# Kernel optimization log

Measured on AMD Instinct MI355X. Metric: run time of the kernel, lower is better.

Reference implementation:

```python
import jax, jax.numpy as jnp
import numpy as np
from jax import lax

DIM = 384
HEADS = 8
CROP = 8


def conv2d(x, w, groups=1, pad=0):
    return lax.conv_general_dilated(
        x, w, (1, 1), ((pad, pad), (pad, pad)),
        dimension_numbers=("NCHW", "OIHW", "NCHW"),
        feature_group_count=groups)


def l2norm(x, axis):
    # F.normalize: x / max(||x||_2, 1e-12)
    n = jnp.sqrt(jnp.sum(x * x, axis=axis, keepdims=True))
    return x / jnp.maximum(n, 1e-12)


def masked_softmax(a, k):
    # top-k mask via k-th largest threshold (equivalent to scatter mask for
    # continuous-valued scores), then softmax with -inf fill.
    kth = lax.top_k(a, k)[0][..., -1:]
    return jax.nn.softmax(jnp.where(a >= kth, a, -jnp.inf), axis=-1)


def setup_inputs() -> dict:
    key = jax.random.key(0)
    ks = jax.random.split(key, 5)
    b, c, h, w = 2, DIM, 128, 128
    x = jax.random.normal(ks[0], (b, c, h, w), dtype=jnp.float32)
    w_qkv = jax.random.normal(ks[1], (3 * c, c, 1, 1), dtype=jnp.float32) * 0.02
    w_dw = jax.random.normal(ks[2], (3 * c, 1, 3, 3), dtype=jnp.float32) * 0.02
    w_proj = jax.random.normal(ks[3], (c, c, 1, 1), dtype=jnp.float32) * 0.02
    temperature = jnp.ones((HEADS, 1, 1), dtype=jnp.float32)
    a = jnp.full((1,), 0.2, dtype=jnp.float32)
    return {"x": x, "w_qkv": w_qkv, "w_dw": w_dw, "w_proj": w_proj,
            "temperature": temperature, "attn1": a, "attn2": a,
            "attn3": a, "attn4": a}


def reference(x, w_qkv, w_dw, w_proj, temperature, attn1, attn2, attn3, attn4):
    b, c, h, w = x.shape
    heads, crop = HEADS, CROP
    ch = c // heads                      # per-head channels C
    N = crop * crop                      # window tokens

    qkv = conv2d(conv2d(x, w_qkv), w_dw, groups=3 * c, pad=1)
    q, k, v = jnp.split(qkv, 3, axis=1)

    def to_heads(t):                     # b (head c) h w -> b head c (h w)
        return t.reshape(b, heads, ch, h * w)

    def to_win(t):                       # imgtowindows on (b, head, c, h, w)
        t = t.reshape(b, heads, ch, h // crop, crop, w // crop, crop)
        t = jnp.transpose(t, (0, 1, 3, 5, 4, 6, 2))
        return t.reshape(-1, heads, N, ch)

    qc, kc, vc = to_heads(q), to_heads(k), to_heads(v)
    qs = to_win(q.reshape(b, heads, ch, h, w))
    ks_ = to_win(k.reshape(b, heads, ch, h, w))
    vs = to_win(v.reshape(b, heads, ch, h, w))

    qc, kc = l2norm(qc, -1), l2norm(kc, -1)
    qs, ks_ = l2norm(qs, -1), l2norm(ks_, -1)

    cattn = jnp.einsum("bhcn,bhdn->bhcd", qc, kc) * temperature  # (b,H,C,C)
    sattn = jnp.einsum("bhnc,bhmc->bhnm", qs, ks_) * temperature  # (B',H,N,N)

    cks = [ch // 2, (ch * 2) // 3, (ch * 3) // 4, (ch * 4) // 5]
    sks = [N // 2, (N * 2) // 3, (N * 3) // 4, (N * 4) // 5]
    wts = [attn1, attn2, attn3, attn4]

    cout = sum((masked_softmax(cattn, kk) @ vc) * wt for kk, wt in zip(cks, wts))
    sout = sum((masked_softmax(sattn, kk) @ vs) * wt for kk, wt in zip(sks, wts))

    # windowstoimg (replicates torch's contiguous view/reshape semantics)
    sout = sout.reshape(b, heads, h, w, ch)
    sout = jnp.transpose(sout, (0, 1, 4, 2, 3)).reshape(b, heads, ch, h * w)

    out = (sout + cout).reshape(b, c, h, w)
    return conv2d(out, w_proj)
```

## Files before the change

### kernel.cpp

```cpp
#include <hip/hip_runtime.h>
#include <hip/hip_bf16.h>


#define HW 16384
#define CDIM 384
#define NHEADS 8
#define CH 48
#define NCHUNK 128

typedef __hip_bfloat16 bf16;
typedef __attribute__((ext_vector_type(8))) short short8;
typedef __attribute__((ext_vector_type(4))) float f32x4;

static __device__ __forceinline__ unsigned short f2bf_bits(float v) {
  bf16 b = __float2bfloat16(v);
  return __builtin_bit_cast(unsigned short, b);
}
static __device__ __forceinline__ float bfbits2f(unsigned short u) {
  return __bfloat162float(__builtin_bit_cast(bf16, u));
}

template <int CTRL>
static __device__ __forceinline__ float dppf(float x) {
  return __builtin_bit_cast(
      float, __builtin_amdgcn_update_dpp(0, __builtin_bit_cast(int, x), CTRL,
                                         0xF, 0xF, true));
}

__global__ __launch_bounds__(256) void decomp_w(const float* __restrict__ src,
                                                unsigned short* __restrict__ h,
                                                unsigned short* __restrict__ l, int n) {
  int i = blockIdx.x * 256 + threadIdx.x;
  if (i >= n) return;
  float v = src[i];
  unsigned short hb = f2bf_bits(v);
  h[i] = hb;
  l[i] = f2bf_bits(v - bfbits2f(hb));
}

__global__ __launch_bounds__(256) void transpose_frag(const float* __restrict__ src,
                                                      short8* __restrict__ dh,
                                                      short8* __restrict__ dl) {
  const int o = blockIdx.x * 256 + threadIdx.x;
  const int ptile = o / 768;
  const int rem = o - ptile * 768;
  const int kc = rem >> 6, lane = rem & 63;
  const int p = ptile * 16 + (lane & 15);
  const int kb = kc * 32 + (lane >> 4) * 8;
  short8 hh, ll;
#pragma unroll
  for (int j = 0; j < 8; j++) {
    float v = src[(size_t)(kb + j) * HW + p];
    unsigned short hb = f2bf_bits(v);
    hh[j] = (short)hb;
    ll[j] = (short)f2bf_bits(v - bfbits2f(hb));
  }
  dh[o] = hh;
  dl[o] = ll;
}

__global__ __launch_bounds__(256, 4) void gemm_mfma(const unsigned short* __restrict__ Wh,
                                                    const unsigned short* __restrict__ Wl,
                                                    const short8* __restrict__ Xh,
                                                    const short8* __restrict__ Xl,
                                                    float* __restrict__ Out) {
  const int tid = threadIdx.x;
  const int wave = tid >> 6, lane = tid & 63;
  const int lm = lane & 15, lq = lane >> 4;
  const int g = blockIdx.y * 128 + blockIdx.x;
  const int xcd = g & 7, i = g >> 3;
  const int bx = xcd * 16 + (i & 15);
  const int by = i >> 4;
  const int p0 = bx * 128;
  const int oc0 = by * 64;
  const int pt0 = bx * 8 + wave * 2;
  f32x4 acc[4][2] = {};
#pragma unroll
  for (int kc = 0; kc < 12; kc++) {
    short8 ah[4], al[4], bh[2], bl[2];
#pragma unroll
    for (int mt = 0; mt < 4; mt++) {
      const size_t off = (size_t)(oc0 + mt * 16 + lm) * 384 + kc * 32 + lq * 8;
      ah[mt] = *reinterpret_cast<const short8*>(Wh + off);
      al[mt] = *reinterpret_cast<const short8*>(Wl + off);
    }
#pragma unroll
    for (int nt = 0; nt < 2; nt++) {
      const size_t idx = (size_t)((pt0 + nt) * 12 + kc) * 64 + lane;
      bh[nt] = Xh[idx];
      bl[nt] = Xl[idx];
    }
#pragma unroll
    for (int mt = 0; mt < 4; mt++)
#pragma unroll
      for (int nt = 0; nt < 2; nt++) {
        acc[mt][nt] = __builtin_amdgcn_mfma_f32_16x16x32_bf16(ah[mt], bh[nt], acc[mt][nt], 0, 0, 0);
        acc[mt][nt] = __builtin_amdgcn_mfma_f32_16x16x32_bf16(ah[mt], bl[nt], acc[mt][nt], 0, 0, 0);
        acc[mt][nt] = __builtin_amdgcn_mfma_f32_16x16x32_bf16(al[mt], bh[nt], acc[mt][nt], 0, 0, 0);
      }
  }
#pragma unroll
  for (int mt = 0; mt < 4; mt++)
#pragma unroll
    for (int nt = 0; nt < 2; nt++)
#pragma unroll
      for (int r = 0; r < 4; r++) {
        const int oc = oc0 + mt * 16 + lq * 4 + r;
        const int p = p0 + (wave * 2 + nt) * 16 + lm;
        Out[(size_t)oc * HW + p] = acc[mt][nt][r];
      }
}

__global__ __launch_bounds__(256) void dwconv3(const float* __restrict__ A,
                                               const float* __restrict__ wdw,
                                               float* __restrict__ Bq) {
  const int e = blockIdx.x * 256 + threadIdx.x;
  const int x4 = e & 31;
  const int y = (e >> 5) & 127;
  const int ch = e >> 12;
  const int x0 = x4 << 2;
  float w[9];
#pragma unroll
  for (int t = 0; t < 9; t++) w[t] = wdw[ch * 9 + t];
  const float* Ap = A + (size_t)ch * HW;
  float4 acc = {0.f, 0.f, 0.f, 0.f};
#pragma unroll
  for (int ky = 0; ky < 3; ky++) {
    const int yy = y + ky - 1;
    if (yy < 0 || yy > 127) continue;
    const float* row = Ap + yy * 128;
    const float4 c = *(const float4*)(row + x0);
    const float l = (x4 == 0) ? 0.f : row[x0 - 1];
    const float r = (x4 == 31) ? 0.f : row[x0 + 4];
    const float w0 = w[ky * 3], w1 = w[ky * 3 + 1], w2 = w[ky * 3 + 2];
    acc.x += w0 * l + w1 * c.x + w2 * c.y;
    acc.y += w0 * c.x + w1 * c.y + w2 * c.z;
    acc.z += w0 * c.y + w1 * c.z + w2 * c.w;
    acc.w += w0 * c.z + w1 * c.w + w2 * r;
  }
  *(float4*)(Bq + (size_t)e * 4) = acc;
}

__global__ __launch_bounds__(256) void chan_norms(const float* __restrict__ Bq,
                                                  float* __restrict__ inv) {
  const int row = blockIdx.x;
  const float4* base = (const float4*)(Bq + (size_t)row * HW);
  const int tid = threadIdx.x;
  float s = 0.f;
  for (int p = tid; p < HW / 4; p += 256) {
    const float4 v = base[p];
    s += v.x * v.x + v.y * v.y + v.z * v.z + v.w * v.w;
  }
  for (int o = 32; o; o >>= 1) s += __shfl_xor(s, o);
  __shared__ float red[4];
  if ((tid & 63) == 0) red[tid >> 6] = s;
  __syncthreads();
  if (tid == 0) {
    float t = red[0] + red[1] + red[2] + red[3];
    inv[row] = 1.f / fmaxf(sqrtf(t), 1e-12f);
  }
}

__global__ __launch_bounds__(256, 3) void cattn_partial(const float* __restrict__ Bq,
                                                        float* __restrict__ part) {
  __shared__ __align__(16) float qs[48 * 132];
  __shared__ __align__(16) float ks2[48 * 132];
  const int tid = threadIdx.x;
  const int chunk = blockIdx.x, h = blockIdx.y;
  const int p0 = chunk * 128;
#pragma unroll
  for (int i = 0; i < 12; i++) {
    const int s4 = tid + i * 256;
    const int t = s4 >= 1536;
    const int r4 = s4 - t * 1536;
    const int cc = r4 >> 5;
    const int px = (r4 & 31) << 2;
    const float4 v4 = *(const float4*)(Bq + (size_t)(t * CDIM + h * CH + cc) * HW + p0 + px);
    *(float4*)((t ? ks2 : qs) + cc * 132 + px) = v4;
  }
  __syncthreads();
  const int tx = tid & 15, ty = tid >> 4;
  const float* qb = qs + (ty * 3) * 132;
  const float* kb = ks2 + (tx * 3) * 132;
  float acc[3][3] = {};
  for (int pl = 0; pl < 128; pl += 4) {
    float4 qv[3], kv[3];
#pragma unroll
    for (int ii = 0; ii < 3; ii++) qv[ii] = *(const float4*)(qb + ii * 132 + pl);
#pragma unroll
    for (int jj = 0; jj < 3; jj++) kv[jj] = *(const float4*)(kb + jj * 132 + pl);
#pragma unroll
    for (int ii = 0; ii < 3; ii++)
#pragma unroll
      for (int jj = 0; jj < 3; jj++)
        acc[ii][jj] += qv[ii].x * kv[jj].x + qv[ii].y * kv[jj].y +
                       qv[ii].z * kv[jj].z + qv[ii].w * kv[jj].w;
  }
  float* rp = part + (size_t)(h * NCHUNK + chunk) * 2304;
#pragma unroll
  for (int ii = 0; ii < 3; ii++)
#pragma unroll
    for (int jj = 0; jj < 3; jj++)
      rp[(ty * 3 + ii) * 48 + tx * 3 + jj] = acc[ii][jj];
}

__global__ __launch_bounds__(64) void chan_softmax(
    const float* __restrict__ part, const float* __restrict__ inv,
    const float* __restrict__ temp, const float* __restrict__ a1,
    const float* __restrict__ a2, const float* __restrict__ a3,
    const float* __restrict__ a4, float* __restrict__ W48) {
  const int blk = blockIdx.x;
  const int i = blk % 48;
  const int h = blk / 48;
  const int lane = threadIdx.x;
  const float t = temp[h];
  float a = -3.0e38f;
  if (lane < 48) {
    const float* pp = part + (size_t)h * NCHUNK * 2304 + i * 48 + lane;
    float r = 0.f;
#pragma unroll 8
    for (int c = 0; c < NCHUNK; c++) r += pp[(size_t)c * 2304];
    a = t * inv[h * CH + i] * inv[CDIM + h * CH + lane] * r;
  }
  float m = a;
  for (int o = 32; o; o >>= 1) m = fmaxf(m, __shfl_xor(m, o));
  float e = (lane < 48) ? expf(a - m) : 0.f;
  int gt = 0;
  for (int j = 0; j < 48; j++) {
    float vj = __shfl(a, j);
    gt += (vj > a) ? 1 : 0;
  }
  const int ksel[4] = {24, 32, 36, 38};
  const float wts[4] = {a1[0], a2[0], a3[0], a4[0]};
  float coef = 0.f;
#pragma unroll
  for (int kk = 0; kk < 4; kk++) {
    float sel = (gt < ksel[kk]) ? e : 0.f;
    for (int o = 32; o; o >>= 1) sel += __shfl_xor(sel, o);
    if (gt < ksel[kk]) coef += wts[kk] / sel;
  }
  if (lane < 48) W48[(size_t)blk * 48 + lane] = e * coef;
}

__global__ __launch_bounds__(256) void cout_kernel(const float* __restrict__ W48,
                                                   const float* __restrict__ Bq,
                                                   float* __restrict__ Cbuf) {
  __shared__ __align__(16) float Wl[2304];
  const int tid = threadIdx.x;
  const int h = blockIdx.y;
  const float* wsrc = W48 + (size_t)h * 2304;
  for (int s = tid; s < 2304; s += 256) Wl[s] = wsrc[s];
  __syncthreads();
  const int p = blockIdx.x * 64 + (tid & 63);
  const int ig = tid >> 6;
  const float* vbase = Bq + (size_t)(2 * CDIM + h * CH) * HW + p;
  float acc[12] = {};
  for (int j0 = 0; j0 < 48; j0 += 4) {
    float vj[4];
#pragma unroll
    for (int q = 0; q < 4; q++) vj[q] = vbase[(size_t)(j0 + q) * HW];
#pragma unroll
    for (int ii = 0; ii < 12; ii++) {
      const float4 w4 = *reinterpret_cast<const float4*>(&Wl[(ig * 12 + ii) * 48 + j0]);
      acc[ii] += w4.x * vj[0] + w4.y * vj[1] + w4.z * vj[2] + w4.w * vj[3];
    }
  }
  float* obase = Cbuf + (size_t)(h * CH + ig * 12) * HW + p;
#pragma unroll
  for (int ii = 0; ii < 12; ii++) obase[(size_t)ii * HW] += acc[ii];
}

static __device__ __forceinline__ void conv_frag_k(int f, const float* kRaw,
                                                   short8* KFh, short8* KFl) {
  int nt, ks, slot;
  if (f < 256) { nt = f >> 6; ks = 0; slot = f & 63; }
  else { const int g2 = f - 256; nt = g2 >> 5; ks = 1; slot = g2 & 31; }
  const int tok = nt * 16 + (slot & 15);
  const int ch0 = ks * 32 + (slot >> 4) * 8;
  const float* src = kRaw + tok * 49 + ch0;
  short8 hh, ll;
#pragma unroll
  for (int j = 0; j < 8; j++) {
    const float v = src[j];
    const unsigned short hb = f2bf_bits(v);
    hh[j] = (short)hb;
    ll[j] = (short)f2bf_bits(v - bfbits2f(hb));
  }
  KFh[f] = hh;
  KFl[f] = ll;
}

__global__ __launch_bounds__(256, 4) void spatial_kernel(
    const float* __restrict__ Bq, const float* __restrict__ temp,
    const float* __restrict__ a1, const float* __restrict__ a2,
    const float* __restrict__ a3, const float* __restrict__ a4,
    float* __restrict__ Cbuf) {
  __shared__ __align__(16) char smem[40192];
  float* qRaw = (float*)smem;
  float* kRaw = (float*)(smem + 12544);
  short8* KFh = (short8*)(smem + 25088);
  short8* KFl = (short8*)(smem + 31232);
  float* S_lds = (float*)smem;
  unsigned short* VTh = (unsigned short*)(smem + 16640);
  unsigned short* VTl = (unsigned short*)(smem + 23552);
  bf16* Pl = (bf16*)(smem + 30464);
  float* O_lds = (float*)smem;
  float* invQ = (float*)(smem + 39680);
  float* invK = (float*)(smem + 39936);

  const int bid = blockIdx.x;
  const int wid = ((bid & 7) << 8) | (bid >> 3);
  const int wx = wid & 15, wy = (wid >> 4) & 15;
  const int head = wid >> 8;
  const int tid = threadIdx.x;
  const int lane = tid & 63, w = tid >> 6;
  const int lm = lane & 15, lq = lane >> 4;
  const int ybase = wy * 8, xbase = wx * 8;
  const size_t hb = (size_t)(head * CH) * HW;

#pragma unroll
  for (int i = 0; i < 6; i++) {
    const int s4 = tid + i * 256;
    const int t = s4 >= 768;
    const int r4 = s4 - t * 768;
    const int cc = r4 >> 4, nq = r4 & 15;
    const int n = nq * 4;
    const int y = ybase + (n >> 3), x = xbase + (n & 7);
    const float4 v4 = *(const float4*)(Bq + (size_t)(t * CDIM) * HW + hb +
                                       (size_t)cc * HW + y * 128 + x);
    float* dst = (t ? kRaw : qRaw) + n * 49 + cc;
    dst[0] = v4.x; dst[49] = v4.y; dst[98] = v4.z; dst[147] = v4.w;
  }
  __syncthreads();

  float4 vv[3];
#pragma unroll
  for (int i = 0; i < 3; i++) {
    const int e4 = tid + i * 256;
    const int cc = e4 >> 4, n = (e4 & 15) * 4;
    const int y = ybase + (n >> 3), x = xbase + (n & 7);
    vv[i] = *(const float4*)(Bq + (size_t)(2 * CDIM) * HW + hb +
                             (size_t)cc * HW + y * 128 + x);
  }

  if (tid < 128) {
    const int t = tid >> 6, n = tid & 63;
    const float* src = (t ? kRaw : qRaw) + n * 49;
    float ssum = 0.f;
#pragma unroll
    for (int cc = 0; cc < 48; cc++) { float v = src[cc]; ssum += v * v; }
    const float iv = 1.f / fmaxf(sqrtf(ssum), 1e-12f);
    if (t) invK[n] = iv; else invQ[n] = iv * temp[head];
  }

  conv_frag_k(tid, kRaw, KFh, KFl);
  if (tid < 128) conv_frag_k(256 + tid, kRaw, KFh, KFl);

  short8 qh[2], ql[2];
#pragma unroll
  for (int ks = 0; ks < 2; ks++) {
    const int ch0 = ks * 32 + lq * 8;
    const float* qp = qRaw + (w * 16 + lm) * 49 + ch0;
#pragma unroll
    for (int j = 0; j < 8; j++) {
      const float v = (ch0 < 48) ? qp[j] : 0.f;
      const unsigned short hbts = f2bf_bits(v);
      qh[ks][j] = (short)hbts;
      ql[ks][j] = (short)f2bf_bits(v - bfbits2f(hbts));
    }
  }
  __syncthreads();

  f32x4 sacc[4] = {};
#pragma unroll
  for (int nt = 0; nt < 4; nt++) {
    const short8 kh0 = KFh[nt * 64 + lane];
    const short8 kl0 = KFl[nt * 64 + lane];
    sacc[nt] = __builtin_amdgcn_mfma_f32_16x16x32_bf16(qh[0], kh0, sacc[nt], 0, 0, 0);
    sacc[nt] = __builtin_amdgcn_mfma_f32_16x16x32_bf16(qh[0], kl0, sacc[nt], 0, 0, 0);
    sacc[nt] = __builtin_amdgcn_mfma_f32_16x16x32_bf16(ql[0], kh0, sacc[nt], 0, 0, 0);
    short8 kh1 = {0, 0, 0, 0, 0, 0, 0, 0}, kl1 = {0, 0, 0, 0, 0, 0, 0, 0};
    if (lane < 32) { kh1 = KFh[256 + nt * 32 + lane]; kl1 = KFl[256 + nt * 32 + lane]; }
    sacc[nt] = __builtin_amdgcn_mfma_f32_16x16x32_bf16(qh[1], kh1, sacc[nt], 0, 0, 0);
    sacc[nt] = __builtin_amdgcn_mfma_f32_16x16x32_bf16(qh[1], kl1, sacc[nt], 0, 0, 0);
    sacc[nt] = __builtin_amdgcn_mfma_f32_16x16x32_bf16(ql[1], kh1, sacc[nt], 0, 0, 0);
  }

  float iqv[4];
#pragma unroll
  for (int r = 0; r < 4; r++) iqv[r] = invQ[w * 16 + lq * 4 + r];
#pragma unroll
  for (int nt = 0; nt < 4; nt++) {
    const float ik = invK[nt * 16 + lm];
#pragma unroll
    for (int r = 0; r < 4; r++)
      S_lds[(w * 16 + lq * 4 + r) * 65 + nt * 16 + lm] = sacc[nt][r] * iqv[r] * ik;
  }
  __syncthreads();

#pragma unroll
  for (int i = 0; i < 3; i++) {
    const int e4 = tid + i * 256;
    const int cc = e4 >> 4, n = (e4 & 15) * 4;
    const float v0 = vv[i].x, v1 = vv[i].y, v2 = vv[i].z, v3 = vv[i].w;
    const unsigned short h0 = f2bf_bits(v0), h1 = f2bf_bits(v1),
                         h2 = f2bf_bits(v2), h3 = f2bf_bits(v3);
    const ushort4 hh = {h0, h1, h2, h3};
    const ushort4 ll = {f2bf_bits(v0 - bfbits2f(h0)), f2bf_bits(v1 - bfbits2f(h1)),
                        f2bf_bits(v2 - bfbits2f(h2)), f2bf_bits(v3 - bfbits2f(h3))};
    *(ushort4*)(VTh + cc * 72 + n) = hh;
    *(ushort4*)(VTl + cc * 72 + n) = ll;
  }

  const float wts[4] = {a1[0], a2[0], a3[0], a4[0]};
  const int sidx[4] = {32, 22, 16, 13};
#pragma unroll 4
  for (int rr = 0; rr < 16; rr++) {
    const int row = w * 16 + rr;
    const float a = S_lds[row * 65 + lane];
    float s = a;
#pragma unroll
    for (int k2 = 2; k2 <= 64; k2 <<= 1) {
#pragma unroll
      for (int j = k2 >> 1; j > 0; j >>= 1) {
        float o;
        if (j == 1)      o = dppf<0xB1>(s);
        else if (j == 2) o = dppf<0x4E>(s);
        else if (j == 8) o = dppf<0x128>(s);
        else             o = __shfl_xor(s, j);
        const bool up = ((lane & k2) == 0);
        const bool lower = ((lane & j) == 0);
        const float mn = fminf(s, o), mx = fmaxf(s, o);
        s = (lower == up) ? mn : mx;
      }
    }
    const float m = __shfl(s, 63);
    float v = __expf(s - m);
    v += dppf<0x101>(v);
    v += dppf<0x102>(v);
    v += dppf<0x104>(v);
    v += dppf<0x108>(v);
    const float t1 = __shfl(v, 16), t2 = __shfl(v, 32), t3 = __shfl(v, 48);
    const float beyond =
        (lq == 0) ? (t1 + t2 + t3) : (lq == 1) ? (t2 + t3) : (lq == 2) ? t3 : 0.f;
    const float suf = v + beyond;
    const float e = __expf(a - m);
    float coef = 0.f;
#pragma unroll
    for (int kk = 0; kk < 4; kk++) {
      const float tk = __shfl(s, sidx[kk]);
      const float Sk = __shfl(suf, sidx[kk]);
      if (a >= tk) coef += wts[kk] * __builtin_amdgcn_rcpf(Sk);
    }
    Pl[row * 72 + lane] = __float2bfloat16(e * coef);
  }
  __syncthreads();

  short8 pa[2];
#pragma unroll
  for (int ks = 0; ks < 2; ks++)
    pa[ks] = *reinterpret_cast<const short8*>(&Pl[(w * 16 + lm) * 72 + ks * 32 + lq * 8]);
  f32x4 oacc[3] = {};
#pragma unroll
  for (int nt = 0; nt < 3; nt++) {
    const int chv = nt * 16 + lm;
#pragma unroll
    for (int ks = 0; ks < 2; ks++) {
      const short8 vh = *reinterpret_cast<const short8*>(VTh + chv * 72 + ks * 32 + lq * 8);
      const short8 vl = *reinterpret_cast<const short8*>(VTl + chv * 72 + ks * 32 + lq * 8);
      oacc[nt] = __builtin_amdgcn_mfma_f32_16x16x32_bf16(pa[ks], vh, oacc[nt], 0, 0, 0);
      oacc[nt] = __builtin_amdgcn_mfma_f32_16x16x32_bf16(pa[ks], vl, oacc[nt], 0, 0, 0);
    }
  }
#pragma unroll
  for (int nt = 0; nt < 3; nt++)
#pragma unroll
    for (int r = 0; r < 4; r++)
      O_lds[(nt * 16 + lm) * 65 + w * 16 + lq * 4 + r] = oacc[nt][r];
  __syncthreads();

  const int y_out = wy * 8 + (wx >> 1);
  const int x0 = (wx & 1) * 64;
#pragma unroll
  for (int i = 0; i < 3; i++) {
    const int s4 = tid + i * 256;
    const int cc = s4 >> 4, n = (s4 & 15) * 4;
    const float* op = O_lds + cc * 65 + n;
    const float4 o4 = {op[0], op[1], op[2], op[3]};
    *(float4*)(Cbuf + ((size_t)(head * CH + cc) * 128 + y_out) * 128 + x0 + n) = o4;
  }
}

extern "C" void kernel_launch(void* const* d_in, const int* in_sizes, int n_in,
                              void* d_out, int out_size, void* d_ws, size_t ws_size,
                              hipStream_t stream) {
  const float* x = (const float*)d_in[0];
  const float* w_qkv = (const float*)d_in[1];
  const float* w_dw = (const float*)d_in[2];
  const float* w_proj = (const float*)d_in[3];
  const float* temp = (const float*)d_in[4];
  const float* a1 = (const float*)d_in[5];
  const float* a2 = (const float*)d_in[6];
  const float* a3 = (const float*)d_in[7];
  const float* a4 = (const float*)d_in[8];
  float* out = (float*)d_out;

  char* ws = (char*)d_ws;
  float* cattn_part = (float*)ws;
  float* W48 = (float*)(ws + 9437184);
  float* inv = (float*)(ws + 9510912);
  unsigned short* wqkv_h = (unsigned short*)(ws + 9513984);
  unsigned short* wqkv_l = (unsigned short*)(ws + 10398720);
  unsigned short* wproj_h = (unsigned short*)(ws + 11283456);
  unsigned short* wproj_l = (unsigned short*)(ws + 11578368);
  float* Bq = (float*)(ws + 11873280);
  short8* Xtgh = (short8*)(ws + 11873280 + (size_t)2 * CDIM * HW * 4);
  short8* Xtgl = (short8*)(ws + 11873280 + (size_t)2 * CDIM * HW * 4 + 12582912);
  short8* Ctgh = (short8*)(ws + 11873280);
  short8* Ctgl = (short8*)(ws + 11873280 + 12582912);

  decomp_w<<<(3 * CDIM * CDIM + 255) / 256, 256, 0, stream>>>(w_qkv, wqkv_h, wqkv_l,
                                                              3 * CDIM * CDIM);
  decomp_w<<<(CDIM * CDIM + 255) / 256, 256, 0, stream>>>(w_proj, wproj_h, wproj_l,
                                                          CDIM * CDIM);

  for (int b = 0; b < 2; b++) {
    const float* xb = x + (size_t)b * CDIM * HW;
    float* ob = out + (size_t)b * CDIM * HW;

    transpose_frag<<<3072, 256, 0, stream>>>(xb, Xtgh, Xtgl);
    for (int t = 0; t < 3; t++) {
      gemm_mfma<<<dim3(HW / 128, CDIM / 64), 256, 0, stream>>>(
          wqkv_h + (size_t)t * CDIM * CDIM, wqkv_l + (size_t)t * CDIM * CDIM,
          Xtgh, Xtgl, ob);
      dwconv3<<<(CDIM * HW / 4) / 256, 256, 0, stream>>>(
          ob, w_dw + (size_t)t * CDIM * 9, Bq + (size_t)t * CDIM * HW);
    }

    chan_norms<<<2 * CDIM, 256, 0, stream>>>(Bq, inv);
    cattn_partial<<<dim3(NCHUNK, NHEADS), 256, 0, stream>>>(Bq, cattn_part);
    chan_softmax<<<NHEADS * 48, 64, 0, stream>>>(cattn_part, inv, temp, a1, a2, a3, a4, W48);
    spatial_kernel<<<NHEADS * 256, 256, 0, stream>>>(Bq, temp, a1, a2, a3, a4, ob);
    cout_kernel<<<dim3(HW / 64, NHEADS), 256, 0, stream>>>(W48, Bq, ob);

    transpose_frag<<<3072, 256, 0, stream>>>(ob, Ctgh, Ctgl);
    gemm_mfma<<<dim3(HW / 128, CDIM / 64), 256, 0, stream>>>(wproj_h, wproj_l,
                                                             Ctgh, Ctgl, ob);
  }

  (void)in_sizes; (void)n_in; (void)out_size; (void)ws_size;
}
```

Before: 804.5 us.

## Fuse channel norms into cattn_partial and channel-attention output into spatial kernel

Drops the separate chan_norms pass by accumulating per-channel sum of squares with atomics inside cattn_partial, using the tiles it already holds in LDS, and zeroing the accumulator in transpose_frag. Drops cout_kernel by loading the per-head 48x48 channel-attention weights into the spatial kernel as bf16 hi/lo fragments and adding W·V through extra MFMAs into the same output accumulators. This saves full passes over Bq and the read-modify-write of the output buffer. In exchange the spatial kernel uses more LDS, its occupancy bound drops from 4 to 3, and float atomics make the norm sums order-dependent.

```diff
diff --git a/kernel.cpp b/kernel.cpp
--- a/kernel.cpp
+++ b/kernel.cpp
@@ -40,7 +40,12 @@
 
 __global__ __launch_bounds__(256) void transpose_frag(const float* __restrict__ src,
                                                       short8* __restrict__ dh,
-                                                      short8* __restrict__ dl) {
+                                                      short8* __restrict__ dl,
+                                                      float* __restrict__ sumsq) {
+  if (blockIdx.x == 0 && threadIdx.x < 192) {
+    const float4 z = {0.f, 0.f, 0.f, 0.f};
+    ((float4*)sumsq)[threadIdx.x] = z;
+  }
   const int o = blockIdx.x * 256 + threadIdx.x;
   const int ptile = o / 768;
   const int rem = o - ptile * 768;
@@ -141,28 +146,9 @@
   *(float4*)(Bq + (size_t)e * 4) = acc;
 }
 
-__global__ __launch_bounds__(256) void chan_norms(const float* __restrict__ Bq,
-                                                  float* __restrict__ inv) {
-  const int row = blockIdx.x;
-  const float4* base = (const float4*)(Bq + (size_t)row * HW);
-  const int tid = threadIdx.x;
-  float s = 0.f;
-  for (int p = tid; p < HW / 4; p += 256) {
-    const float4 v = base[p];
-    s += v.x * v.x + v.y * v.y + v.z * v.z + v.w * v.w;
-  }
-  for (int o = 32; o; o >>= 1) s += __shfl_xor(s, o);
-  __shared__ float red[4];
-  if ((tid & 63) == 0) red[tid >> 6] = s;
-  __syncthreads();
-  if (tid == 0) {
-    float t = red[0] + red[1] + red[2] + red[3];
-    inv[row] = 1.f / fmaxf(sqrtf(t), 1e-12f);
-  }
-}
-
 __global__ __launch_bounds__(256, 3) void cattn_partial(const float* __restrict__ Bq,
-                                                        float* __restrict__ part) {
+                                                        float* __restrict__ part,
+                                                        float* __restrict__ sumsq) {
   __shared__ __align__(16) float qs[48 * 132];
   __shared__ __align__(16) float ks2[48 * 132];
   const int tid = threadIdx.x;
@@ -179,6 +165,18 @@
     *(float4*)((t ? ks2 : qs) + cc * 132 + px) = v4;
   }
   __syncthreads();
+  if (tid < 96) {
+    const int t = tid >= 48;
+    const int cc = t ? tid - 48 : tid;
+    const float* src = (t ? ks2 : qs) + cc * 132;
+    float s = 0.f;
+#pragma unroll
+    for (int p = 0; p < 128; p += 4) {
+      const float4 v = *(const float4*)(src + p);
+      s += v.x * v.x + v.y * v.y + v.z * v.z + v.w * v.w;
+    }
+    atomicAdd(&sumsq[t * CDIM + h * CH + cc], s);
+  }
   const int tx = tid & 15, ty = tid >> 4;
   const float* qb = qs + (ty * 3) * 132;
   const float* kb = ks2 + (tx * 3) * 132;
@@ -205,7 +203,7 @@
 }
 
 __global__ __launch_bounds__(64) void chan_softmax(
-    const float* __restrict__ part, const float* __restrict__ inv,
+    const float* __restrict__ part, const float* __restrict__ sumsq,
     const float* __restrict__ temp, const float* __restrict__ a1,
     const float* __restrict__ a2, const float* __restrict__ a3,
     const float* __restrict__ a4, float* __restrict__ W48) {
@@ -220,7 +218,9 @@
     float r = 0.f;
 #pragma unroll 8
     for (int c = 0; c < NCHUNK; c++) r += pp[(size_t)c * 2304];
-    a = t * inv[h * CH + i] * inv[CDIM + h * CH + lane] * r;
+    const float iq = 1.f / fmaxf(sqrtf(sumsq[h * CH + i]), 1e-12f);
+    const float ik = 1.f / fmaxf(sqrtf(sumsq[CDIM + h * CH + lane]), 1e-12f);
+    a = t * iq * ik * r;
   }
   float m = a;
   for (int o = 32; o; o >>= 1) m = fmaxf(m, __shfl_xor(m, o));
@@ -240,34 +240,6 @@
     if (gt < ksel[kk]) coef += wts[kk] / sel;
   }
   if (lane < 48) W48[(size_t)blk * 48 + lane] = e * coef;
-}
-
-__global__ __launch_bounds__(256) void cout_kernel(const float* __restrict__ W48,
-                                                   const float* __restrict__ Bq,
-                                                   float* __restrict__ Cbuf) {
-  __shared__ __align__(16) float Wl[2304];
-  const int tid = threadIdx.x;
-  const int h = blockIdx.y;
-  const float* wsrc = W48 + (size_t)h * 2304;
-  for (int s = tid; s < 2304; s += 256) Wl[s] = wsrc[s];
-  __syncthreads();
-  const int p = blockIdx.x * 64 + (tid & 63);
-  const int ig = tid >> 6;
-  const float* vbase = Bq + (size_t)(2 * CDIM + h * CH) * HW + p;
-  float acc[12] = {};
-  for (int j0 = 0; j0 < 48; j0 += 4) {
-    float vj[4];
-#pragma unroll
-    for (int q = 0; q < 4; q++) vj[q] = vbase[(size_t)(j0 + q) * HW];
-#pragma unroll
-    for (int ii = 0; ii < 12; ii++) {
-      const float4 w4 = *reinterpret_cast<const float4*>(&Wl[(ig * 12 + ii) * 48 + j0]);
-      acc[ii] += w4.x * vj[0] + w4.y * vj[1] + w4.z * vj[2] + w4.w * vj[3];
-    }
-  }
-  float* obase = Cbuf + (size_t)(h * CH + ig * 12) * HW + p;
-#pragma unroll
-  for (int ii = 0; ii < 12; ii++) obase[(size_t)ii * HW] += acc[ii];
 }
 
 static __device__ __forceinline__ void conv_frag_k(int f, const float* kRaw,
@@ -289,13 +261,30 @@
   KFh[f] = hh;
   KFl[f] = ll;
 }
-
-__global__ __launch_bounds__(256, 4) void spatial_kernel(
-    const float* __restrict__ Bq, const float* __restrict__ temp,
-    const float* __restrict__ a1, const float* __restrict__ a2,
-    const float* __restrict__ a3, const float* __restrict__ a4,
-    float* __restrict__ Cbuf) {
-  __shared__ __align__(16) char smem[40192];
+static __device__ __forceinline__ void conv_frag_w(int f, const float* __restrict__ wsrc,
+                                                   short8* WFh, short8* WFl) {
+  int nt, n, k0;
+  if (f < 192) { nt = f >> 6; const int slot = f & 63; n = slot & 15; k0 = (slot >> 4) * 8; }
+  else { const int g2 = f - 192; nt = g2 >> 5; const int slot = g2 & 31; n = slot & 15; k0 = 32 + (slot >> 4) * 8; }
+  const float* src = wsrc + (nt * 16 + n) * 48 + k0;
+  short8 hh, ll;
+#pragma unroll
+  for (int j = 0; j < 8; j++) {
+    const float v = src[j];
+    const unsigned short hb = f2bf_bits(v);
+    hh[j] = (short)hb;
+    ll[j] = (short)f2bf_bits(v - bfbits2f(hb));
+  }
+  WFh[f] = hh;
+  WFl[f] = ll;
+}
+
+__global__ __launch_bounds__(256, 3) void spatial_kernel(
+    const float* __restrict__ Bq, const float* __restrict__ W48,
+    const float* __restrict__ temp, const float* __restrict__ a1,
+    const float* __restrict__ a2, const float* __restrict__ a3,
+    const float* __restrict__ a4, float* __restrict__ Cbuf) {
+  __shared__ __align__(16) char smem[49408];
   float* qRaw = (float*)smem;
   float* kRaw = (float*)(smem + 12544);
   short8* KFh = (short8*)(smem + 25088);
@@ -304,9 +293,13 @@
   unsigned short* VTh = (unsigned short*)(smem + 16640);
   unsigned short* VTl = (unsigned short*)(smem + 23552);
   bf16* Pl = (bf16*)(smem + 30464);
-  float* O_lds = (float*)smem;
-  float* invQ = (float*)(smem + 39680);
-  float* invK = (float*)(smem + 39936);
+  unsigned short* V2h = (unsigned short*)smem;
+  unsigned short* V2l = (unsigned short*)(smem + 8192);
+  short8* WFh = (short8*)(smem + 39680);
+  short8* WFl = (short8*)(smem + 44288);
+  float* O_lds = (float*)(smem + 16640);
+  float* invQ = (float*)(smem + 48896);
+  float* invK = (float*)(smem + 49152);
 
   const int bid = blockIdx.x;
   const int wid = ((bid & 7) << 8) | (bid >> 3);
@@ -316,6 +309,8 @@
   const int lane = tid & 63, w = tid >> 6;
   const int lm = lane & 15, lq = lane >> 4;
   const int ybase = wy * 8, xbase = wx * 8;
+  const int y_out = wy * 8 + (wx >> 1);
+  const int x0 = (wx & 1) * 64;
   const size_t hb = (size_t)(head * CH) * HW;
 
 #pragma unroll
@@ -331,9 +326,11 @@
     float* dst = (t ? kRaw : qRaw) + n * 49 + cc;
     dst[0] = v4.x; dst[49] = v4.y; dst[98] = v4.z; dst[147] = v4.w;
   }
-  __syncthreads();
-
-  float4 vv[3];
+  conv_frag_w(tid, W48 + (size_t)head * 2304, WFh, WFl);
+  if (tid < 32) conv_frag_w(256 + tid, W48 + (size_t)head * 2304, WFh, WFl);
+  __syncthreads();
+
+  float4 vv[3], vc[3];
 #pragma unroll
   for (int i = 0; i < 3; i++) {
     const int e4 = tid + i * 256;
@@ -341,6 +338,8 @@
     const int y = ybase + (n >> 3), x = xbase + (n & 7);
     vv[i] = *(const float4*)(Bq + (size_t)(2 * CDIM) * HW + hb +
                              (size_t)cc * HW + y * 128 + x);
+    vc[i] = *(const float4*)(Bq + (size_t)(2 * CDIM) * HW + hb +
+                             (size_t)cc * HW + y_out * 128 + x0 + n);
   }
 
   if (tid < 128) {
@@ -456,10 +455,42 @@
   }
   __syncthreads();
 
+#pragma unroll
+  for (int i = 0; i < 3; i++) {
+    const int e4 = tid + i * 256;
+    const int cc = e4 >> 4, n0 = (e4 & 15) * 4;
+#pragma unroll
+    for (int dt = 0; dt < 4; dt++) {
+      const int tok = n0 + dt;
+      const float v = (dt == 0) ? vc[i].x : (dt == 1) ? vc[i].y
+                     : (dt == 2) ? vc[i].z : vc[i].w;
+      const unsigned short hv = f2bf_bits(v);
+      const int col = ((((cc >> 3) ^ (tok & 7)) << 3) | (cc & 7));
+      V2h[tok * 64 + col] = hv;
+      V2l[tok * 64 + col] = f2bf_bits(v - bfbits2f(hv));
+    }
+  }
+  {
+    const int buf = tid >> 7, r2 = tid & 127;
+    const int tok = r2 >> 1, jbl = 6 + (r2 & 1);
+    const int phys = (jbl ^ (tok & 7)) << 3;
+    const short8 z = {0, 0, 0, 0, 0, 0, 0, 0};
+    *(short8*)((buf ? V2l : V2h) + tok * 64 + phys) = z;
+  }
+  __syncthreads();
+
   short8 pa[2];
 #pragma unroll
   for (int ks = 0; ks < 2; ks++)
     pa[ks] = *reinterpret_cast<const short8*>(&Pl[(w * 16 + lm) * 72 + ks * 32 + lq * 8]);
+  const int tokA = w * 16 + lm;
+  short8 a2h[2], a2l[2];
+#pragma unroll
+  for (int ks = 0; ks < 2; ks++) {
+    const int phys = (((ks * 4 + lq) ^ (lm & 7)) << 3);
+    a2h[ks] = *reinterpret_cast<const short8*>(V2h + tokA * 64 + phys);
+    a2l[ks] = *reinterpret_cast<const short8*>(V2l + tokA * 64 + phys);
+  }
   f32x4 oacc[3] = {};
 #pragma unroll
   for (int nt = 0; nt < 3; nt++) {
@@ -471,7 +502,21 @@
       oacc[nt] = __builtin_amdgcn_mfma_f32_16x16x32_bf16(pa[ks], vh, oacc[nt], 0, 0, 0);
       oacc[nt] = __builtin_amdgcn_mfma_f32_16x16x32_bf16(pa[ks], vl, oacc[nt], 0, 0, 0);
     }
-  }
+    {
+      const short8 wh0 = WFh[nt * 64 + lane];
+      const short8 wl0 = WFl[nt * 64 + lane];
+      oacc[nt] = __builtin_amdgcn_mfma_f32_16x16x32_bf16(a2h[0], wh0, oacc[nt], 0, 0, 0);
+      oacc[nt] = __builtin_amdgcn_mfma_f32_16x16x32_bf16(a2h[0], wl0, oacc[nt], 0, 0, 0);
+      oacc[nt] = __builtin_amdgcn_mfma_f32_16x16x32_bf16(a2l[0], wh0, oacc[nt], 0, 0, 0);
+      short8 wh1 = {0, 0, 0, 0, 0, 0, 0, 0}, wl1 = {0, 0, 0, 0, 0, 0, 0, 0};
+      if (lane < 32) { wh1 = WFh[192 + nt * 32 + lane]; wl1 = WFl[192 + nt * 32 + lane]; }
+      oacc[nt] = __builtin_amdgcn_mfma_f32_16x16x32_bf16(a2h[1], wh1, oacc[nt], 0, 0, 0);
+      oacc[nt] = __builtin_amdgcn_mfma_f32_16x16x32_bf16(a2h[1], wl1, oacc[nt], 0, 0, 0);
+      oacc[nt] = __builtin_amdgcn_mfma_f32_16x16x32_bf16(a2l[1], wh1, oacc[nt], 0, 0, 0);
+    }
+  }
+  __syncthreads();
+
 #pragma unroll
   for (int nt = 0; nt < 3; nt++)
 #pragma unroll
@@ -479,8 +524,6 @@
       O_lds[(nt * 16 + lm) * 65 + w * 16 + lq * 4 + r] = oacc[nt][r];
   __syncthreads();
 
-  const int y_out = wy * 8 + (wx >> 1);
-  const int x0 = (wx & 1) * 64;
 #pragma unroll
   for (int i = 0; i < 3; i++) {
     const int s4 = tid + i * 256;
@@ -508,7 +551,7 @@
   char* ws = (char*)d_ws;
   float* cattn_part = (float*)ws;
   float* W48 = (float*)(ws + 9437184);
-  float* inv = (float*)(ws + 9510912);
+  float* sumsq = (float*)(ws + 9510912);
   unsigned short* wqkv_h = (unsigned short*)(ws + 9513984);
   unsigned short* wqkv_l = (unsigned short*)(ws + 10398720);
   unsigned short* wproj_h = (unsigned short*)(ws + 11283456);
@@ -528,7 +571,7 @@
     const float* xb = x + (size_t)b * CDIM * HW;
     float* ob = out + (size_t)b * CDIM * HW;
 
-    transpose_frag<<<3072, 256, 0, stream>>>(xb, Xtgh, Xtgl);
+    transpose_frag<<<3072, 256, 0, stream>>>(xb, Xtgh, Xtgl, sumsq);
     for (int t = 0; t < 3; t++) {
       gemm_mfma<<<dim3(HW / 128, CDIM / 64), 256, 0, stream>>>(
           wqkv_h + (size_t)t * CDIM * CDIM, wqkv_l + (size_t)t * CDIM * CDIM,
@@ -537,13 +580,11 @@
           ob, w_dw + (size_t)t * CDIM * 9, Bq + (size_t)t * CDIM * HW);
     }
 
-    chan_norms<<<2 * CDIM, 256, 0, stream>>>(Bq, inv);
-    cattn_partial<<<dim3(NCHUNK, NHEADS), 256, 0, stream>>>(Bq, cattn_part);
-    chan_softmax<<<NHEADS * 48, 64, 0, stream>>>(cattn_part, inv, temp, a1, a2, a3, a4, W48);
-    spatial_kernel<<<NHEADS * 256, 256, 0, stream>>>(Bq, temp, a1, a2, a3, a4, ob);
-    cout_kernel<<<dim3(HW / 64, NHEADS), 256, 0, stream>>>(W48, Bq, ob);
-
-    transpose_frag<<<3072, 256, 0, stream>>>(ob, Ctgh, Ctgl);
+    cattn_partial<<<dim3(NCHUNK, NHEADS), 256, 0, stream>>>(Bq, cattn_part, sumsq);
+    chan_softmax<<<NHEADS * 48, 64, 0, stream>>>(cattn_part, sumsq, temp, a1, a2, a3, a4, W48);
+    spatial_kernel<<<NHEADS * 256, 256, 0, stream>>>(Bq, W48, temp, a1, a2, a3, a4, ob);
+
+    transpose_frag<<<3072, 256, 0, stream>>>(ob, Ctgh, Ctgl, sumsq);
     gemm_mfma<<<dim3(HW / 128, CDIM / 64), 256, 0, stream>>>(wproj_h, wproj_l,
                                                              Ctgh, Ctgl, ob);
   }
```

New measurement: 757.2 us. 5.9% less time.
